# Kernel tuning notes

Hardware: AMD Instinct MI355X
Metric: run time of the kernel (lower is better)

## Reference

```python
import jax, jax.numpy as jnp
import numpy as np

N = 256          # batch size
C = 100          # nb_classes
D = 512          # sz_embed
SCALE = 3.0
EPS = 1e-12      # F.normalize eps
M = N * (N - 1) // 2  # number of (i<j) candidate pairs


def l2norm(x):
    # matches F.normalize(p=2, dim=-1) with eps=1e-12
    return x / jnp.maximum(jnp.linalg.norm(x, axis=-1, keepdims=True), EPS)


def dist_block(A, B):
    # squared euclidean distance block of pairwise_distance(cat([A,B]))[0][:len(A), len(A):]
    # (off-diagonal block, so the eye-masking in the original is a no-op; negatives zeroed)
    d = (A * A).sum(-1, keepdims=True) + (B * B).sum(-1)[None, :] - 2.0 * (A @ B.T)
    return jnp.maximum(d, 0.0)


def setup_inputs() -> dict:
    key = jax.random.key(0)
    k1, k2, k3 = jax.random.split(key, 3)
    X = jax.random.normal(k1, (N, D), dtype=jnp.float32)
    proxies = jax.random.normal(k2, (C, D), dtype=jnp.float32) / 8.0
    T = jax.random.randint(k3, (N,), 0, C)
    indices = jnp.arange(N)  # unused by forward, kept for signature fidelity
    return {"X": X, "proxies": proxies, "T": T, "indices": indices}


def reference(X, proxies, T, indices):
    Pn = SCALE * l2norm(proxies)           # (C, D)
    Xn = SCALE * l2norm(X)                 # (N, D)
    IP = Xn @ Pn.T                         # (N, C) inner-product block

    # --- intercls_mixup (method=1, uncertainty-guided lambdas) ---
    # all i<j pairs; same-class pairs are masked out (original skips them in a Python loop)
    i1, i2 = jnp.triu_indices(N, k=1)      # (M,), (M,)
    diff = T[i1] != T[i2]                  # (M,) valid cross-class pairs
    c1, c2 = T[i1], T[i2]

    X1P1 = jnp.clip(IP[i1, c1], -1.0, 1.0)
    X1P2 = jnp.clip(IP[i1, c2], -1.0, 1.0)
    X2P1 = jnp.clip(IP[i2, c1], -1.0, 1.0)
    X2P2 = jnp.clip(IP[i2, c2], -1.0, 1.0)
    lam = jnp.clip((X2P2 - X2P1) / (X2P2 - X2P1 + X1P1 - X1P2), 0.3, 0.7)
    lam = jnp.where(diff, lam, 0.5)        # neutralize masked (same-class) pairs

    virt = lam[:, None] * Xn[i1] + (1.0 - lam[:, None]) * Xn[i2]  # (M, D)
    virt = l2norm(virt)

    # --- proxy-NCA loss over real + virtual samples ---
    Xall = jnp.concatenate([Xn, SCALE * virt], axis=0)            # (N+M, D)
    Dall = dist_block(Xall, Pn)                                   # (N+M, C)
    logsm = jax.nn.log_softmax(-Dall, axis=-1)

    loss_real = -logsm[jnp.arange(N), T]                          # one-hot targets
    lv = logsm[N:]                                                # (M, C)
    rows = jnp.arange(M)
    # virtual soft targets: lam*onehot(c1) + (1-lam)*onehot(c2)
    loss_virt = -(lam * lv[rows, c1] + (1.0 - lam) * lv[rows, c2])

    total = loss_real.sum() + jnp.sum(jnp.where(diff, loss_virt, 0.0))
    count = N + diff.sum()
    return total / count
```

## Files before the change

### kernel.cpp

```cpp
#include <hip/hip_runtime.h>
#include <hip/hip_bf16.h>
#include <math.h>

#define N_ 256
#define C_ 100
#define D_ 512
#define LOG2E 1.44269504088896f

#define WS_GX  0
#define WS_GTP 65536
#define WS_RN  91136

typedef __attribute__((ext_vector_type(8))) short short8;
typedef __attribute__((ext_vector_type(4))) float floatx4;

__device__ inline float waveReduceSum(float v) {
    #pragma unroll
    for (int off = 32; off > 0; off >>= 1) v += __shfl_xor(v, off, 64);
    return v;
}
__device__ inline float clip1(float x) { return fminf(fmaxf(x, -1.0f), 1.0f); }

__device__ inline short8 cvt8(float4 a, float4 b) {
    union { __hip_bfloat16 h[8]; short8 s; } u;
    u.h[0] = __float2bfloat16(a.x); u.h[1] = __float2bfloat16(a.y);
    u.h[2] = __float2bfloat16(a.z); u.h[3] = __float2bfloat16(a.w);
    u.h[4] = __float2bfloat16(b.x); u.h[5] = __float2bfloat16(b.y);
    u.h[6] = __float2bfloat16(b.z); u.h[7] = __float2bfloat16(b.w);
    return u.s;
}

__global__ __launch_bounds__(256)
void gemm_kernel(const float* __restrict__ X, const float* __restrict__ P,
                 float* __restrict__ ws) {
    float* Gx  = ws + WS_GX;
    float* GTP = ws + WS_GTP;
    float* rn  = ws + WS_RN;
    __shared__ floatx4 accl[3][64];
    int tile = blockIdx.x;
    int t = threadIdx.x, w = t >> 6, lane = t & 63;
    int r = lane & 15, quad = lane >> 4;
    const float *arow, *brow;
    int tm, tn, mode;
    if (tile < 136) {
        mode = 0;
        int u = tile; tm = 0;
        while (u >= 16 - tm) { u -= 16 - tm; ++tm; }
        tn = tm + u;
        arow = X + (size_t)(tm * 16 + r) * D_;
        brow = X + (size_t)(tn * 16 + r) * D_;
    } else if (tile < 248) {
        int u = tile - 136; mode = 1; tm = u / 7; tn = u - tm * 7;
        int pb = tn * 16 + r; if (pb >= C_) pb = 0;
        arow = X + (size_t)(tm * 16 + r) * D_;
        brow = P + (size_t)pb * D_;
    } else {
        mode = 2; tm = tile - 248; tn = tm;
        int pa = tm * 16 + r; if (pa >= C_) pa = 0;
        arow = P + (size_t)pa * D_;
        brow = arow;
    }
    floatx4 acc = {0.0f, 0.0f, 0.0f, 0.0f};
    int k0 = w * 128;
    #pragma unroll
    for (int kk = 0; kk < 128; kk += 32) {
        const float4* ap = (const float4*)(arow + k0 + kk + quad * 8);
        const float4* bp = (const float4*)(brow + k0 + kk + quad * 8);
        short8 av = cvt8(ap[0], ap[1]);
        short8 bv = cvt8(bp[0], bp[1]);
        acc = __builtin_amdgcn_mfma_f32_16x16x32_bf16(av, bv, acc, 0, 0, 0);
    }
    if (w) accl[w - 1][lane] = acc;
    __syncthreads();
    if (w == 0) {
        acc += accl[0][lane]; acc += accl[1][lane]; acc += accl[2][lane];
        if (mode == 0) {
            int row0 = tm * 16 + quad * 4, col = tn * 16 + r;
            #pragma unroll
            for (int i = 0; i < 4; ++i) Gx[(row0 + i) * 256 + col] = acc[i];
            if (tm == tn && (r >> 2) == quad)
                rn[tm * 16 + r] = 3.0f * rsqrtf(fmaxf(acc[r & 3], 1e-24f));
        } else if (mode == 1) {
            int c = tn * 16 + r;
            if (c < C_) {
                int row0 = tm * 16 + quad * 4;
                #pragma unroll
                for (int i = 0; i < 4; ++i)
                    GTP[(c >> 2) * 1024 + (row0 + i) * 4 + (c & 3)] = acc[i];
            }
        } else {
            if ((r >> 2) == quad) {
                int pr = tm * 16 + r;
                if (pr < C_) rn[256 + pr] = 3.0f * rsqrtf(fmaxf(acc[r & 3], 1e-24f));
            }
        }
    }
}

__global__ __launch_bounds__(1024)
void pair_kernel(const float* __restrict__ ws, const int* __restrict__ T,
                 float* __restrict__ out) {
    const float* Gx   = ws + WS_GX;
    const float4* G4  = (const float4*)(ws + WS_GTP);
    const float* GTPf = ws + WS_GTP;
    const float* rn   = ws + WS_RN;
    __shared__ __attribute__((aligned(16))) float wbufA[16][104];
    __shared__ __attribute__((aligned(16))) float wbufS[16][104];
    __shared__ int hist[C_];
    __shared__ float red[16];

    int t = threadIdx.x, w = t >> 6, lane = t & 63;
    int b = blockIdx.x;
    int m = t >> 2, p = t & 3;

    int t1 = T[b];
    int t2 = T[m];
    float s1 = rn[b], sc2 = rn[m];
    float graw = 0.0f;
    if (m >= b) graw = Gx[b * 256 + m];
    float4 a2r[7];
    #pragma unroll
    for (int k = 0; k < 7; ++k) {
        int q = p + 4 * k;
        a2r[k] = (float4){0.f, 0.f, 0.f, 0.f};
        if (q < 25 && m >= b) a2r[k] = G4[q * 256 + m];
    }
    int Tt = (t < 256) ? T[t] : 0;
    if (t < C_) hist[t] = 0;
    if (lane < 25) {
        float4 av = G4[lane * 256 + b];
        float4 sv = *(const float4*)(rn + 256 + lane * 4);
        *(float4*)&wbufA[w][lane * 4] = av;
        *(float4*)&wbufS[w][lane * 4] = sv;
    }

    bool diag = (m == b);
    bool act = diag || ((m > b) && (t2 != t1));
    float contrib = 0.0f;
    if (act) {
        float ip11r = wbufA[w][t1], ip12r = wbufA[w][t2];
        float sp1 = wbufS[w][t1], sp2 = wbufS[w][t2];
        float ip21r = GTPf[(t1 >> 2) * 1024 + m * 4 + (t1 & 3)];
        float ip22r = GTPf[(t2 >> 2) * 1024 + m * 4 + (t2 & 3)];
        float ip11 = ip11r * s1 * sp1, ip12 = ip12r * s1 * sp2;
        float ip21 = ip21r * sc2 * sp1, ip22 = ip22r * sc2 * sp2;
        float X1P1 = clip1(ip11), X1P2 = clip1(ip12);
        float X2P1 = clip1(ip21), X2P2 = clip1(ip22);
        float num = X2P2 - X2P1;
        float den = num + X1P1 - X1P2;
        float lam = fminf(fmaxf(num / den, 0.3f), 0.7f);
        if (diag) lam = 1.0f;
        float oml = 1.0f - lam;
        float g = graw * s1 * sc2;
        float wn2 = 9.0f * (lam * lam + oml * oml) + 2.0f * lam * oml * g;
        float ss2 = 6.0f * rsqrtf(fmaxf(wn2, 1e-24f));
        float la = ss2 * lam * s1 * LOG2E, lb = ss2 * oml * sc2 * LOG2E;
        float sm = 0.0f;
        #pragma unroll
        for (int k = 0; k < 7; ++k) {
            int q = p + 4 * k;
            if (q < 25) {
                float4 a1 = *(const float4*)&wbufA[w][q * 4];
                float4 s4 = *(const float4*)&wbufS[w][q * 4];
                float4 a2 = a2r[k];
                sm += exp2f(s4.x * (la * a1.x + lb * a2.x));
                sm += exp2f(s4.y * (la * a1.y + lb * a2.y));
                sm += exp2f(s4.z * (la * a1.z + lb * a2.z));
                sm += exp2f(s4.w * (la * a1.w + lb * a2.w));
            }
        }
        sm += __shfl_xor(sm, 1, 64);
        sm += __shfl_xor(sm, 2, 64);
        if (p == 0) {
            float LSE = logf(sm);
            float ec1 = ss2 * (lam * ip11 + oml * ip21);
            float ec2 = ss2 * (lam * ip12 + oml * ip22);
            contrib = LSE - lam * ec1 - oml * ec2;
        }
    }
    float rsum = waveReduceSum(contrib);
    if (lane == 0) red[w] = rsum;
    __syncthreads();
    if (t < 256) atomicAdd(&hist[Tt], 1);
    __syncthreads();
    if (w == 0) {
        float same;
        { float n = (float)hist[lane]; same = 0.5f * n * (n - 1.0f); }
        if (lane + 64 < C_) { float n = (float)hist[lane + 64]; same += 0.5f * n * (n - 1.0f); }
        float bs = (lane < 16) ? red[lane] : 0.0f;
        same = waveReduceSum(same);
        bs = waveReduceSum(bs);
        if (lane == 0) atomicAdd(out, bs / (32896.0f - same));
    }
}

extern "C" void kernel_launch(void* const* d_in, const int* in_sizes, int n_in,
                              void* d_out, int out_size, void* d_ws, size_t ws_size,
                              hipStream_t stream) {
    const float* X = (const float*)d_in[0];
    const float* P = (const float*)d_in[1];
    const int*   T = (const int*)d_in[2];
    float* ws = (float*)d_ws;
    float* out = (float*)d_out;

    gemm_kernel<<<255, 256, 0, stream>>>(X, P, ws);
    pair_kernel<<<N_, 1024, 0, stream>>>(ws, T, out);
}
```

Before: 69.44 us.

## Fold proxy norms into GEMM epilogue and split K across 16 waves

The GEMM kernel now runs 1024 threads per tile, with each of 16 waves doing a single 32-wide K slice. This replaces 4 waves that each looped over 128. Proxy row norms are computed in fp32 from the loaded B operand and applied to the X·P tile before storing, so the separate proxy-norm tiles and the scale buffer are dropped. The pair kernel therefore skips the per-class scale loads and multiplies in its exp loop, hoists the two GTP gathers, and splits the exp sum across four accumulators. The cost is a larger shared-memory reduction over 15 partial accumulators per tile and more threads per block.

```diff
diff --git a/kernel.cpp b/kernel.cpp
--- a/kernel.cpp
+++ b/kernel.cpp
@@ -30,13 +30,14 @@
     return u.s;
 }
 
-__global__ __launch_bounds__(256)
+__global__ __launch_bounds__(1024)
 void gemm_kernel(const float* __restrict__ X, const float* __restrict__ P,
                  float* __restrict__ ws) {
     float* Gx  = ws + WS_GX;
     float* GTP = ws + WS_GTP;
     float* rn  = ws + WS_RN;
-    __shared__ floatx4 accl[3][64];
+    __shared__ floatx4 accl[15][64];
+    __shared__ float normp[16][16];
     int tile = blockIdx.x;
     int t = threadIdx.x, w = t >> 6, lane = t & 63;
     int r = lane & 15, quad = lane >> 4;
@@ -49,49 +50,47 @@
         tn = tm + u;
         arow = X + (size_t)(tm * 16 + r) * D_;
         brow = X + (size_t)(tn * 16 + r) * D_;
-    } else if (tile < 248) {
+    } else {
         int u = tile - 136; mode = 1; tm = u / 7; tn = u - tm * 7;
         int pb = tn * 16 + r; if (pb >= C_) pb = 0;
         arow = X + (size_t)(tm * 16 + r) * D_;
         brow = P + (size_t)pb * D_;
-    } else {
-        mode = 2; tm = tile - 248; tn = tm;
-        int pa = tm * 16 + r; if (pa >= C_) pa = 0;
-        arow = P + (size_t)pa * D_;
-        brow = arow;
-    }
+    }
+    int k0 = w * 32;
+    const float4* ap = (const float4*)(arow + k0 + quad * 8);
+    const float4* bp = (const float4*)(brow + k0 + quad * 8);
+    float4 a0 = ap[0], a1v = ap[1];
+    float4 b0 = bp[0], b1v = bp[1];
+    short8 av = cvt8(a0, a1v);
+    short8 bv = cvt8(b0, b1v);
     floatx4 acc = {0.0f, 0.0f, 0.0f, 0.0f};
-    int k0 = w * 128;
-    #pragma unroll
-    for (int kk = 0; kk < 128; kk += 32) {
-        const float4* ap = (const float4*)(arow + k0 + kk + quad * 8);
-        const float4* bp = (const float4*)(brow + k0 + kk + quad * 8);
-        short8 av = cvt8(ap[0], ap[1]);
-        short8 bv = cvt8(bp[0], bp[1]);
-        acc = __builtin_amdgcn_mfma_f32_16x16x32_bf16(av, bv, acc, 0, 0, 0);
-    }
+    acc = __builtin_amdgcn_mfma_f32_16x16x32_bf16(av, bv, acc, 0, 0, 0);
+    float s8 = b0.x*b0.x + b0.y*b0.y + b0.z*b0.z + b0.w*b0.w
+             + b1v.x*b1v.x + b1v.y*b1v.y + b1v.z*b1v.z + b1v.w*b1v.w;
+    s8 += __shfl_xor(s8, 16, 64);
+    s8 += __shfl_xor(s8, 32, 64);
+    if (quad == 0) normp[w][r] = s8;
     if (w) accl[w - 1][lane] = acc;
     __syncthreads();
     if (w == 0) {
-        acc += accl[0][lane]; acc += accl[1][lane]; acc += accl[2][lane];
+        #pragma unroll
+        for (int i = 0; i < 15; ++i) acc += accl[i][lane];
+        int row0 = tm * 16 + quad * 4, col = tn * 16 + r;
         if (mode == 0) {
-            int row0 = tm * 16 + quad * 4, col = tn * 16 + r;
             #pragma unroll
             for (int i = 0; i < 4; ++i) Gx[(row0 + i) * 256 + col] = acc[i];
             if (tm == tn && (r >> 2) == quad)
                 rn[tm * 16 + r] = 3.0f * rsqrtf(fmaxf(acc[r & 3], 1e-24f));
-        } else if (mode == 1) {
-            int c = tn * 16 + r;
+        } else {
+            float cn = 0.0f;
+            #pragma unroll
+            for (int i = 0; i < 16; ++i) cn += normp[i][r];
+            float spc = 3.0f * rsqrtf(fmaxf(cn, 1e-24f));
+            int c = col;
             if (c < C_) {
-                int row0 = tm * 16 + quad * 4;
                 #pragma unroll
                 for (int i = 0; i < 4; ++i)
-                    GTP[(c >> 2) * 1024 + (row0 + i) * 4 + (c & 3)] = acc[i];
-            }
-        } else {
-            if ((r >> 2) == quad) {
-                int pr = tm * 16 + r;
-                if (pr < C_) rn[256 + pr] = 3.0f * rsqrtf(fmaxf(acc[r & 3], 1e-24f));
+                    GTP[(c >> 2) * 1024 + (row0 + i) * 4 + (c & 3)] = acc[i] * spc;
             }
         }
     }
@@ -105,7 +104,6 @@
     const float* GTPf = ws + WS_GTP;
     const float* rn   = ws + WS_RN;
     __shared__ __attribute__((aligned(16))) float wbufA[16][104];
-    __shared__ __attribute__((aligned(16))) float wbufS[16][104];
     __shared__ int hist[C_];
     __shared__ float red[16];
 
@@ -125,25 +123,21 @@
         a2r[k] = (float4){0.f, 0.f, 0.f, 0.f};
         if (q < 25 && m >= b) a2r[k] = G4[q * 256 + m];
     }
+    float u2t1 = GTPf[(t1 >> 2) * 1024 + m * 4 + (t1 & 3)];
+    float u2t2 = GTPf[(t2 >> 2) * 1024 + m * 4 + (t2 & 3)];
     int Tt = (t < 256) ? T[t] : 0;
     if (t < C_) hist[t] = 0;
     if (lane < 25) {
         float4 av = G4[lane * 256 + b];
-        float4 sv = *(const float4*)(rn + 256 + lane * 4);
         *(float4*)&wbufA[w][lane * 4] = av;
-        *(float4*)&wbufS[w][lane * 4] = sv;
     }
 
     bool diag = (m == b);
     bool act = diag || ((m > b) && (t2 != t1));
     float contrib = 0.0f;
     if (act) {
-        float ip11r = wbufA[w][t1], ip12r = wbufA[w][t2];
-        float sp1 = wbufS[w][t1], sp2 = wbufS[w][t2];
-        float ip21r = GTPf[(t1 >> 2) * 1024 + m * 4 + (t1 & 3)];
-        float ip22r = GTPf[(t2 >> 2) * 1024 + m * 4 + (t2 & 3)];
-        float ip11 = ip11r * s1 * sp1, ip12 = ip12r * s1 * sp2;
-        float ip21 = ip21r * sc2 * sp1, ip22 = ip22r * sc2 * sp2;
+        float ip11 = wbufA[w][t1] * s1, ip12 = wbufA[w][t2] * s1;
+        float ip21 = u2t1 * sc2,        ip22 = u2t2 * sc2;
         float X1P1 = clip1(ip11), X1P2 = clip1(ip12);
         float X2P1 = clip1(ip21), X2P2 = clip1(ip22);
         float num = X2P2 - X2P1;
@@ -155,20 +149,20 @@
         float wn2 = 9.0f * (lam * lam + oml * oml) + 2.0f * lam * oml * g;
         float ss2 = 6.0f * rsqrtf(fmaxf(wn2, 1e-24f));
         float la = ss2 * lam * s1 * LOG2E, lb = ss2 * oml * sc2 * LOG2E;
-        float sm = 0.0f;
+        float sm0 = 0.0f, sm1 = 0.0f, sm2 = 0.0f, sm3 = 0.0f;
         #pragma unroll
         for (int k = 0; k < 7; ++k) {
             int q = p + 4 * k;
             if (q < 25) {
                 float4 a1 = *(const float4*)&wbufA[w][q * 4];
-                float4 s4 = *(const float4*)&wbufS[w][q * 4];
                 float4 a2 = a2r[k];
-                sm += exp2f(s4.x * (la * a1.x + lb * a2.x));
-                sm += exp2f(s4.y * (la * a1.y + lb * a2.y));
-                sm += exp2f(s4.z * (la * a1.z + lb * a2.z));
-                sm += exp2f(s4.w * (la * a1.w + lb * a2.w));
+                sm0 += exp2f(la * a1.x + lb * a2.x);
+                sm1 += exp2f(la * a1.y + lb * a2.y);
+                sm2 += exp2f(la * a1.z + lb * a2.z);
+                sm3 += exp2f(la * a1.w + lb * a2.w);
             }
         }
+        float sm = (sm0 + sm1) + (sm2 + sm3);
         sm += __shfl_xor(sm, 1, 64);
         sm += __shfl_xor(sm, 2, 64);
         if (p == 0) {
@@ -203,6 +197,6 @@
     float* ws = (float*)d_ws;
     float* out = (float*)d_out;
 
-    gemm_kernel<<<255, 256, 0, stream>>>(X, P, ws);
+    gemm_kernel<<<248, 1024, 0, stream>>>(X, P, ws);
     pair_kernel<<<N_, 1024, 0, stream>>>(ws, T, out);
 }
```

Result: no change. 69.35 us (-0.1%).
